# Optimization experiments

Measured on AMD Instinct MI355X. Metric: run time of the kernel, lower is better.

## Reference

```python
import jax, jax.numpy as jnp
import numpy as np

NUM_EXPERTS = 8
D_MODEL = 2048
D_FF = 4096
TOP_K = 2
NUM_TOKENS = 4096


def setup_inputs() -> dict:
    key = jax.random.key(0)
    k1, k2, k3, k4, k5, k6 = jax.random.split(key, 6)
    hidden_states = jax.random.normal(k1, (NUM_TOKENS, D_MODEL), dtype=jnp.float32)
    top_k_index = jax.random.randint(k2, (NUM_TOKENS, TOP_K), 0, NUM_EXPERTS)
    raw = jax.random.uniform(k3, (NUM_TOKENS, TOP_K), dtype=jnp.float32)
    top_k_weights = raw / jnp.sum(raw, axis=-1, keepdims=True)  # normalized router weights
    scale = 0.02
    Wg = jax.random.normal(k4, (NUM_EXPERTS, D_MODEL, D_FF), dtype=jnp.float32) * scale
    Wu = jax.random.normal(k5, (NUM_EXPERTS, D_MODEL, D_FF), dtype=jnp.float32) * scale
    Wd = jax.random.normal(k6, (NUM_EXPERTS, D_FF, D_MODEL), dtype=jnp.float32) * scale
    return {
        "hidden_states": hidden_states,
        "top_k_index": top_k_index,
        "top_k_weights": top_k_weights,
        "Wg": Wg,
        "Wu": Wu,
        "Wd": Wd,
    }


def reference(hidden_states, top_k_index, top_k_weights, Wg, Wu, Wd):
    T, D = hidden_states.shape
    E = Wg.shape[0]
    # Combine weights: [T, E], summing duplicate expert hits exactly as the
    # original loop's repeated index_add_ would.
    combine = jnp.zeros((T, E), dtype=top_k_weights.dtype)
    combine = combine.at[jnp.arange(T)[:, None], top_k_index].add(top_k_weights)
    # Dense all-experts SwiGLU (same math per token/expert as the gather loop)
    gate = jnp.einsum("td,edf->tef", hidden_states, Wg)   # [T, E, F]
    up = jnp.einsum("td,edf->tef", hidden_states, Wu)     # [T, E, F]
    h = jax.nn.silu(gate) * up                              # [T, E, F]
    expert_out = jnp.einsum("tef,efd->ted", h, Wd)          # [T, E, D]
    # Weighted scatter-combine
    final = jnp.einsum("ted,te->td", expert_out, combine)   # [T, D]
    return final
```

## Files before the change

kernel.cpp:

```cpp
#include <hip/hip_runtime.h>

#define NTOK 4096
#define DM   2048
#define DF   4096
#define NEXP 8

typedef __attribute__((ext_vector_type(4))) float f32x4;
typedef __attribute__((ext_vector_type(8))) short s16x8;
typedef __attribute__((ext_vector_type(4))) int   i32x4;

__device__ __forceinline__ unsigned short f2bf(float f) {
  union { float f; unsigned u; } x; x.f = f;
  unsigned r = x.u + 0x7fffu + ((x.u >> 16) & 1u);
  return (unsigned short)(r >> 16);
}

__device__ __forceinline__ int swz(int row, int ks) {
  return row * 32 + ((ks ^ ((row >> 1) & 3)) << 3);
}

__global__ void k_zero(int* counts, int* cursor) {
  int i = threadIdx.x;
  if (i < NEXP) { counts[i] = 0; cursor[i] = 0; }
}

__global__ void k_count(const int* __restrict__ idx, int* counts) {
  int t = blockIdx.x * 256 + threadIdx.x;
  if (t >= NTOK) return;
  int e0 = idx[2 * t], e1 = idx[2 * t + 1];
  atomicAdd(&counts[e0], 1);
  if (e1 != e0) atomicAdd(&counts[e1], 1);
}

__global__ void k_scan(const int* __restrict__ counts, int* offsets) {
  if (threadIdx.x == 0) {
    int s = 0;
    for (int e = 0; e < NEXP; e++) { offsets[e] = s; s += counts[e]; }
  }
}

__global__ void k_fill(const int* __restrict__ idx, const float* __restrict__ wts,
                       const int* __restrict__ offsets, int* cursor,
                       int* tokrow, float* wrow, int* rowids) {
  int t = blockIdx.x * 256 + threadIdx.x;
  if (t >= NTOK) return;
  int e0 = idx[2 * t], e1 = idx[2 * t + 1];
  float w0 = wts[2 * t], w1 = wts[2 * t + 1];
  if (e0 == e1) {
    int s = atomicAdd(&cursor[e0], 1);
    int g = offsets[e0] + s;
    tokrow[g] = t; wrow[g] = w0 + w1;
    rowids[2 * t] = g; rowids[2 * t + 1] = -1;
  } else {
    int s0 = atomicAdd(&cursor[e0], 1);
    int g0 = offsets[e0] + s0;
    tokrow[g0] = t; wrow[g0] = w0;
    int s1 = atomicAdd(&cursor[e1], 1);
    int g1 = offsets[e1] + s1;
    tokrow[g1] = t; wrow[g1] = w1;
    rowids[2 * t] = g0; rowids[2 * t + 1] = g1;
  }
}

__global__ __launch_bounds__(512, 2) void gemm1_kernel(
    const float* __restrict__ X, const float* __restrict__ Wg_all,
    const float* __restrict__ Wu_all, const int* __restrict__ counts,
    const int* __restrict__ offsets, const int* __restrict__ tokrow,
    unsigned short* __restrict__ H) {
  const int e = blockIdx.z;
  const int cnt = counts[e];
  const int m0 = blockIdx.y * 256;
  if (m0 >= cnt) return;
  const int n0 = blockIdx.x * 128;
  const int roff = offsets[e];
  const float* __restrict__ Wg = Wg_all + (size_t)e * DM * DF;
  const float* __restrict__ Wu = Wu_all + (size_t)e * DM * DF;

  __shared__ __attribute__((aligned(16))) short As[2][256 * 32];
  __shared__ __attribute__((aligned(16))) short Bs[2][2][128 * 32];

  const int tid = threadIdx.x;
  const int ar  = tid >> 1;
  const int aks = (tid & 1) * 2;
  const int am  = m0 + ar;
  const int atok = (am < cnt) ? tokrow[roff + am] : tokrow[roff];
  const float* __restrict__ xrow = X + (size_t)atok * DM + (tid & 1) * 16;
  const int bmat  = tid >> 8;
  const int bn    = tid & 127;
  const int bktop = ((tid >> 7) & 1) * 16;
  const float* __restrict__ wcol = (bmat ? Wu : Wg) + n0 + bn;

  const int wave = tid >> 6, lane = tid & 63;
  const int wm = wave >> 1, wn = wave & 1;
  const int lr = lane & 15, ks = lane >> 4;

  f32x4 accg[4][4], accu[4][4];
  #pragma unroll
  for (int i = 0; i < 4; i++)
    #pragma unroll
    for (int j = 0; j < 4; j++) {
      accg[i][j] = f32x4{0.f, 0.f, 0.f, 0.f};
      accu[i][j] = f32x4{0.f, 0.f, 0.f, 0.f};
    }

  auto stage = [&](int b, int k0) {
    const f32x4* ap = (const f32x4*)(xrow + k0);
    f32x4 a0 = ap[0], a1 = ap[1], a2 = ap[2], a3 = ap[3];
    float bv[16];
    const float* p = wcol + (size_t)(k0 + bktop) * DF;
    #pragma unroll
    for (int kk = 0; kk < 16; kk++) { bv[kk] = *p; p += DF; }
    s16x8 s;
    #pragma unroll
    for (int j = 0; j < 4; j++) { s[j] = (short)f2bf(a0[j]); s[4 + j] = (short)f2bf(a1[j]); }
    *(s16x8*)&As[b][swz(ar, aks)] = s;
    #pragma unroll
    for (int j = 0; j < 4; j++) { s[j] = (short)f2bf(a2[j]); s[4 + j] = (short)f2bf(a3[j]); }
    *(s16x8*)&As[b][swz(ar, aks + 1)] = s;
    #pragma unroll
    for (int j = 0; j < 8; j++) s[j] = (short)f2bf(bv[j]);
    *(s16x8*)&Bs[b][bmat][swz(bn, bktop >> 3)] = s;
    #pragma unroll
    for (int j = 0; j < 8; j++) s[j] = (short)f2bf(bv[8 + j]);
    *(s16x8*)&Bs[b][bmat][swz(bn, (bktop >> 3) + 1)] = s;
  };

  stage(0, 0);
  __syncthreads();
  int buf = 0;
  const int nK = DM / 32;
  for (int kt = 0; kt < nK; ++kt) {
    if (kt + 1 < nK) stage(buf ^ 1, (kt + 1) * 32);
    s16x8 af[4], bg[4], bu[4];
    #pragma unroll
    for (int mi = 0; mi < 4; mi++)
      af[mi] = *(const s16x8*)&As[buf][swz(wm * 64 + mi * 16 + lr, ks)];
    #pragma unroll
    for (int ni = 0; ni < 4; ni++) {
      bg[ni] = *(const s16x8*)&Bs[buf][0][swz(wn * 64 + ni * 16 + lr, ks)];
      bu[ni] = *(const s16x8*)&Bs[buf][1][swz(wn * 64 + ni * 16 + lr, ks)];
    }
    #pragma unroll
    for (int mi = 0; mi < 4; mi++)
      #pragma unroll
      for (int ni = 0; ni < 4; ni++) {
        accg[mi][ni] = __builtin_amdgcn_mfma_f32_16x16x32_bf16(af[mi], bg[ni], accg[mi][ni], 0, 0, 0);
        accu[mi][ni] = __builtin_amdgcn_mfma_f32_16x16x32_bf16(af[mi], bu[ni], accu[mi][ni], 0, 0, 0);
      }
    __syncthreads();
    buf ^= 1;
  }

  #pragma unroll
  for (int mi = 0; mi < 4; mi++) {
    #pragma unroll
    for (int r = 0; r < 4; r++) {
      int row = wm * 64 + mi * 16 + ks * 4 + r;
      if (m0 + row < cnt) {
        unsigned short* hrow = H + (size_t)(roff + m0 + row) * DF + n0 + wn * 64 + lr;
        #pragma unroll
        for (int ni = 0; ni < 4; ni++) {
          float g = accg[mi][ni][r], u = accu[mi][ni][r];
          float sv = g / (1.f + __expf(-g));
          hrow[ni * 16] = f2bf(sv * u);
        }
      }
    }
  }
}

__global__ __launch_bounds__(512, 2) void gemm2_kernel(
    const unsigned short* __restrict__ H, const float* __restrict__ Wd_all,
    const int* __restrict__ counts, const int* __restrict__ offsets,
    const float* __restrict__ wrow, float* __restrict__ OP) {
  const int e = blockIdx.z;
  const int cnt = counts[e];
  const int m0 = blockIdx.y * 256;
  if (m0 >= cnt) return;
  const int n0 = blockIdx.x * 128;
  const int roff = offsets[e];
  const float* __restrict__ Wd = Wd_all + (size_t)e * DF * DM;

  __shared__ __attribute__((aligned(16))) short As[2][256 * 32];
  __shared__ __attribute__((aligned(16))) short Bs[2][128 * 32];
  __shared__ float wl[256];

  const int tid = threadIdx.x;
  if (tid < 256) wl[tid] = (m0 + tid < cnt) ? wrow[roff + m0 + tid] : 0.f;

  const int ar  = tid >> 1;
  const int aks = (tid & 1) * 2;
  const int am  = m0 + ar;
  const int arow = (am < cnt) ? (roff + am) : roff;
  const unsigned short* __restrict__ hrow = H + (size_t)arow * DF + (tid & 1) * 16;

  const int bn  = tid & 127;
  const int bkg = tid >> 7;
  const float* __restrict__ wcol = Wd + n0 + bn;

  const int wave = tid >> 6, lane = tid & 63;
  const int wm = wave >> 1, wn = wave & 1;
  const int lr = lane & 15, ks = lane >> 4;

  f32x4 acc[4][4];
  #pragma unroll
  for (int i = 0; i < 4; i++)
    #pragma unroll
    for (int j = 0; j < 4; j++) acc[i][j] = f32x4{0.f, 0.f, 0.f, 0.f};

  auto stage = [&](int b, int k0) {
    const i32x4* ap = (const i32x4*)(hrow + k0);
    i32x4 h0 = ap[0], h1 = ap[1];
    float bv[8];
    const float* p = wcol + (size_t)(k0 + bkg * 8) * DM;
    #pragma unroll
    for (int kk = 0; kk < 8; kk++) { bv[kk] = *p; p += DM; }
    *(i32x4*)&As[b][swz(ar, aks)] = h0;
    *(i32x4*)&As[b][swz(ar, aks + 1)] = h1;
    s16x8 s;
    #pragma unroll
    for (int j = 0; j < 8; j++) s[j] = (short)f2bf(bv[j]);
    *(s16x8*)&Bs[b][swz(bn, bkg)] = s;
  };

  stage(0, 0);
  __syncthreads();
  int buf = 0;
  const int nK = DF / 32;
  for (int kt = 0; kt < nK; ++kt) {
    if (kt + 1 < nK) stage(buf ^ 1, (kt + 1) * 32);
    s16x8 af[4], bf_[4];
    #pragma unroll
    for (int mi = 0; mi < 4; mi++)
      af[mi] = *(const s16x8*)&As[buf][swz(wm * 64 + mi * 16 + lr, ks)];
    #pragma unroll
    for (int ni = 0; ni < 4; ni++)
      bf_[ni] = *(const s16x8*)&Bs[buf][swz(wn * 64 + ni * 16 + lr, ks)];
    #pragma unroll
    for (int mi = 0; mi < 4; mi++)
      #pragma unroll
      for (int ni = 0; ni < 4; ni++)
        acc[mi][ni] = __builtin_amdgcn_mfma_f32_16x16x32_bf16(af[mi], bf_[ni], acc[mi][ni], 0, 0, 0);
    __syncthreads();
    buf ^= 1;
  }

  #pragma unroll
  for (int mi = 0; mi < 4; mi++) {
    #pragma unroll
    for (int r = 0; r < 4; r++) {
      int row = wm * 64 + mi * 16 + ks * 4 + r;
      if (m0 + row < cnt) {
        float wgt = wl[row];
        float* orow = OP + (size_t)(roff + m0 + row) * DM + n0 + wn * 64 + lr;
        #pragma unroll
        for (int ni = 0; ni < 4; ni++) orow[ni * 16] = acc[mi][ni][r] * wgt;
      }
    }
  }
}

__global__ void k_combine(const float* __restrict__ OP, const int* __restrict__ rowids,
                          float* __restrict__ out) {
  int gid = blockIdx.x * 256 + threadIdx.x;
  if (gid >= NTOK * DM / 4) return;
  int t = gid >> 9;
  int c = (gid & 511) << 2;
  int r0 = rowids[2 * t], r1 = rowids[2 * t + 1];
  f32x4 v = *(const f32x4*)(OP + (size_t)r0 * DM + c);
  if (r1 >= 0) {
    f32x4 v1 = *(const f32x4*)(OP + (size_t)r1 * DM + c);
    v = v + v1;
  }
  *(f32x4*)(out + (size_t)t * DM + c) = v;
}

extern "C" void kernel_launch(void* const* d_in, const int* in_sizes, int n_in,
                              void* d_out, int out_size, void* d_ws, size_t ws_size,
                              hipStream_t stream) {
  (void)in_sizes; (void)n_in; (void)out_size; (void)ws_size;
  const float* X   = (const float*)d_in[0];
  const int*   idx = (const int*)d_in[1];
  const float* wts = (const float*)d_in[2];
  const float* Wg  = (const float*)d_in[3];
  const float* Wu  = (const float*)d_in[4];
  const float* Wd  = (const float*)d_in[5];
  float* out = (float*)d_out;

  uint8_t* w = (uint8_t*)d_ws;
  int*   counts  = (int*)(w + 0);
  int*   cursor  = (int*)(w + 64);
  int*   offsets = (int*)(w + 128);
  int*   tokrow  = (int*)(w + 256);
  float* wrow    = (float*)(w + 256 + 4 * 8192);
  int*   rowids  = (int*)(w + 256 + 8 * 8192);
  unsigned short* H = (unsigned short*)(w + 131072);
  float* OP = (float*)(w + 131072 + (size_t)8192 * DF * 2);

  k_zero<<<1, 64, 0, stream>>>(counts, cursor);
  k_count<<<16, 256, 0, stream>>>(idx, counts);
  k_scan<<<1, 64, 0, stream>>>(counts, offsets);
  k_fill<<<16, 256, 0, stream>>>(idx, wts, offsets, cursor, tokrow, wrow, rowids);
  gemm1_kernel<<<dim3(DF / 128, 16, NEXP), 512, 0, stream>>>(X, Wg, Wu, counts, offsets, tokrow, H);
  gemm2_kernel<<<dim3(DM / 128, 16, NEXP), 512, 0, stream>>>(H, Wd, counts, offsets, wrow, OP);
  k_combine<<<(NTOK * DM / 4) / 256, 256, 0, stream>>>(OP, rowids, out);
}
```

Measured before the change: 892.1 us.

## Pre-convert weights and gathered X to swizzled bf16 tiles, load via global_load_lds

```diff
diff --git a/kernel.cpp b/kernel.cpp
--- a/kernel.cpp
+++ b/kernel.cpp
@@ -1,26 +1,45 @@
 #include <hip/hip_runtime.h>
+#include <hip/hip_bf16.h>
+#include <stdint.h>
 
 #define NTOK 4096
 #define DM   2048
 #define DF   4096
 #define NEXP 8
+#define NPAD 10240
+#define NPTILE 40
 
 typedef __attribute__((ext_vector_type(4))) float f32x4;
 typedef __attribute__((ext_vector_type(8))) short s16x8;
 typedef __attribute__((ext_vector_type(4))) int   i32x4;
+typedef __attribute__((ext_vector_type(2))) int   i32x2;
 
 __device__ __forceinline__ unsigned short f2bf(float f) {
   union { float f; unsigned u; } x; x.f = f;
   unsigned r = x.u + 0x7fffu + ((x.u >> 16) & 1u);
   return (unsigned short)(r >> 16);
 }
-
+__device__ __forceinline__ unsigned pack2(float lo, float hi) {
+  __hip_bfloat162 h2 = __float22bfloat162_rn(make_float2(lo, hi));
+  return *reinterpret_cast<unsigned*>(&h2);
+}
 __device__ __forceinline__ int swz(int row, int ks) {
   return row * 32 + ((ks ^ ((row >> 1) & 3)) << 3);
 }
-
-__global__ void k_zero(int* counts, int* cursor) {
-  int i = threadIdx.x;
+__device__ __forceinline__ void g2l16(const void* g, void* l) {
+  __builtin_amdgcn_global_load_lds(
+      (const __attribute__((address_space(1))) void*)g,
+      (__attribute__((address_space(3))) void*)l, 16, 0, 0);
+}
+
+__global__ void k_zero_out(float* out) {
+  int gid = blockIdx.x * 256 + threadIdx.x;
+  *(f32x4*)(out + (size_t)gid * 4) = f32x4{0.f, 0.f, 0.f, 0.f};
+}
+
+__global__ void k_init(int* tokrow, int* counts, int* cursor) {
+  int i = blockIdx.x * 256 + threadIdx.x;
+  if (i < NPAD) tokrow[i] = 0;
   if (i < NEXP) { counts[i] = 0; cursor[i] = 0; }
 }
 
@@ -32,67 +51,103 @@
   if (e1 != e0) atomicAdd(&counts[e1], 1);
 }
 
-__global__ void k_scan(const int* __restrict__ counts, int* offsets) {
+__global__ void k_scan(const int* __restrict__ counts, int* poff) {
   if (threadIdx.x == 0) {
     int s = 0;
-    for (int e = 0; e < NEXP; e++) { offsets[e] = s; s += counts[e]; }
+    for (int e = 0; e < NEXP; e++) {
+      poff[e] = s;
+      s += ((counts[e] + 255) & ~255);
+    }
   }
 }
 
 __global__ void k_fill(const int* __restrict__ idx, const float* __restrict__ wts,
-                       const int* __restrict__ offsets, int* cursor,
-                       int* tokrow, float* wrow, int* rowids) {
+                       const int* __restrict__ poff, int* cursor,
+                       int* tokrow, float* wrow) {
   int t = blockIdx.x * 256 + threadIdx.x;
   if (t >= NTOK) return;
   int e0 = idx[2 * t], e1 = idx[2 * t + 1];
   float w0 = wts[2 * t], w1 = wts[2 * t + 1];
   if (e0 == e1) {
-    int s = atomicAdd(&cursor[e0], 1);
-    int g = offsets[e0] + s;
+    int g = poff[e0] + atomicAdd(&cursor[e0], 1);
     tokrow[g] = t; wrow[g] = w0 + w1;
-    rowids[2 * t] = g; rowids[2 * t + 1] = -1;
   } else {
-    int s0 = atomicAdd(&cursor[e0], 1);
-    int g0 = offsets[e0] + s0;
+    int g0 = poff[e0] + atomicAdd(&cursor[e0], 1);
     tokrow[g0] = t; wrow[g0] = w0;
-    int s1 = atomicAdd(&cursor[e1], 1);
-    int g1 = offsets[e1] + s1;
+    int g1 = poff[e1] + atomicAdd(&cursor[e1], 1);
     tokrow[g1] = t; wrow[g1] = w1;
-    rowids[2 * t] = g0; rowids[2 * t + 1] = g1;
-  }
+  }
+}
+
+__global__ void k_convX(const float* __restrict__ X, const int* __restrict__ tokrow,
+                        short* __restrict__ Xg) {
+  const int kt = blockIdx.x, tile = blockIdx.y, tid = threadIdx.x;
+  const int part = tid & 7;
+  short* dst = Xg + (size_t)(tile * 64 + kt) * 8192;
+  #pragma unroll
+  for (int it = 0; it < 8; it++) {
+    int row = it * 32 + (tid >> 3);
+    int tok = tokrow[tile * 256 + row];
+    f32x4 v = *(const f32x4*)(X + (size_t)tok * DM + kt * 32 + part * 4);
+    i32x2 p;
+    p[0] = (int)pack2(v[0], v[1]);
+    p[1] = (int)pack2(v[2], v[3]);
+    int idx = row * 32 + (((part >> 1) ^ ((row >> 1) & 3)) << 3) + (part & 1) * 4;
+    *(i32x2*)&dst[idx] = p;
+  }
+}
+
+__global__ void k_convW(const float* __restrict__ W_all, short* __restrict__ dstbuf,
+                        int e0, int N, int K) {
+  const int nt = blockIdx.x, kt = blockIdx.y, z = blockIdx.z;
+  const int e = e0 + z;
+  const int tid = threadIdx.x;
+  const int kl = tid >> 3, ng = (tid & 7) * 16;
+  const float* src = W_all + (size_t)e * K * N + (size_t)(kt * 32 + kl) * N + nt * 128 + ng;
+
+  __shared__ __attribute__((aligned(16))) short img[4096];
+
+  f32x4 v0 = ((const f32x4*)src)[0];
+  f32x4 v1 = ((const f32x4*)src)[1];
+  f32x4 v2 = ((const f32x4*)src)[2];
+  f32x4 v3 = ((const f32x4*)src)[3];
+  float vv[16];
+  *(f32x4*)&vv[0] = v0; *(f32x4*)&vv[4] = v1;
+  *(f32x4*)&vv[8] = v2; *(f32x4*)&vv[12] = v3;
+  const int ks = kl >> 3, kr = kl & 7;
+  #pragma unroll
+  for (int j = 0; j < 16; j++) {
+    int nl = ng + j;
+    img[nl * 32 + ((ks ^ ((nl >> 1) & 3)) << 3) + kr] = (short)f2bf(vv[j]);
+  }
+  __syncthreads();
+  short* dst = dstbuf + ((size_t)(z * (N / 128) + nt) * (K / 32) + kt) * 4096;
+  *(i32x4*)&dst[tid * 16]     = *(const i32x4*)&img[tid * 16];
+  *(i32x4*)&dst[tid * 16 + 8] = *(const i32x4*)&img[tid * 16 + 8];
 }
 
 __global__ __launch_bounds__(512, 2) void gemm1_kernel(
-    const float* __restrict__ X, const float* __restrict__ Wg_all,
-    const float* __restrict__ Wu_all, const int* __restrict__ counts,
-    const int* __restrict__ offsets, const int* __restrict__ tokrow,
-    unsigned short* __restrict__ H) {
-  const int e = blockIdx.z;
+    const short* __restrict__ Xg, const short* __restrict__ Wgt,
+    const short* __restrict__ Wut, const int* __restrict__ counts,
+    const int* __restrict__ poff, unsigned short* __restrict__ Hs, int e0) {
+  const int z = blockIdx.z, e = e0 + z;
   const int cnt = counts[e];
   const int m0 = blockIdx.y * 256;
   if (m0 >= cnt) return;
-  const int n0 = blockIdx.x * 128;
-  const int roff = offsets[e];
-  const float* __restrict__ Wg = Wg_all + (size_t)e * DM * DF;
-  const float* __restrict__ Wu = Wu_all + (size_t)e * DM * DF;
-
-  __shared__ __attribute__((aligned(16))) short As[2][256 * 32];
-  __shared__ __attribute__((aligned(16))) short Bs[2][2][128 * 32];
-
-  const int tid = threadIdx.x;
-  const int ar  = tid >> 1;
-  const int aks = (tid & 1) * 2;
-  const int am  = m0 + ar;
-  const int atok = (am < cnt) ? tokrow[roff + am] : tokrow[roff];
-  const float* __restrict__ xrow = X + (size_t)atok * DM + (tid & 1) * 16;
-  const int bmat  = tid >> 8;
-  const int bn    = tid & 127;
-  const int bktop = ((tid >> 7) & 1) * 16;
-  const float* __restrict__ wcol = (bmat ? Wu : Wg) + n0 + bn;
-
-  const int wave = tid >> 6, lane = tid & 63;
+  const int nt = blockIdx.x, n0 = nt * 128;
+  const int tileIdx = (poff[e] >> 8) + blockIdx.y;
+
+  __shared__ __attribute__((aligned(16))) short As[2][8192];
+  __shared__ __attribute__((aligned(16))) short Bs[2][2][4096];
+
+  const int tid = threadIdx.x, wave = tid >> 6, lane = tid & 63;
   const int wm = wave >> 1, wn = wave & 1;
   const int lr = lane & 15, ks = lane >> 4;
+  const int bmat = wave >> 2, wv = wave & 3;
+
+  const short* aS = Xg + (size_t)tileIdx * 64 * 8192 + wave * 1024 + lane * 8;
+  const short* bS = (bmat ? Wut : Wgt) + (size_t)(z * 32 + nt) * 64 * 4096
+                    + wv * 1024 + lane * 8;
 
   f32x4 accg[4][4], accu[4][4];
   #pragma unroll
@@ -103,26 +158,11 @@
       accu[i][j] = f32x4{0.f, 0.f, 0.f, 0.f};
     }
 
-  auto stage = [&](int b, int k0) {
-    const f32x4* ap = (const f32x4*)(xrow + k0);
-    f32x4 a0 = ap[0], a1 = ap[1], a2 = ap[2], a3 = ap[3];
-    float bv[16];
-    const float* p = wcol + (size_t)(k0 + bktop) * DF;
-    #pragma unroll
-    for (int kk = 0; kk < 16; kk++) { bv[kk] = *p; p += DF; }
-    s16x8 s;
-    #pragma unroll
-    for (int j = 0; j < 4; j++) { s[j] = (short)f2bf(a0[j]); s[4 + j] = (short)f2bf(a1[j]); }
-    *(s16x8*)&As[b][swz(ar, aks)] = s;
-    #pragma unroll
-    for (int j = 0; j < 4; j++) { s[j] = (short)f2bf(a2[j]); s[4 + j] = (short)f2bf(a3[j]); }
-    *(s16x8*)&As[b][swz(ar, aks + 1)] = s;
-    #pragma unroll
-    for (int j = 0; j < 8; j++) s[j] = (short)f2bf(bv[j]);
-    *(s16x8*)&Bs[b][bmat][swz(bn, bktop >> 3)] = s;
-    #pragma unroll
-    for (int j = 0; j < 8; j++) s[j] = (short)f2bf(bv[8 + j]);
-    *(s16x8*)&Bs[b][bmat][swz(bn, (bktop >> 3) + 1)] = s;
+  auto stage = [&](int b, int kt) {
+    g2l16(aS + (size_t)kt * 8192,       &As[b][wave * 1024]);
+    g2l16(aS + (size_t)kt * 8192 + 512, &As[b][wave * 1024 + 512]);
+    g2l16(bS + (size_t)kt * 4096,       &Bs[b][bmat][wv * 1024]);
+    g2l16(bS + (size_t)kt * 4096 + 512, &Bs[b][bmat][wv * 1024 + 512]);
   };
 
   stage(0, 0);
@@ -130,7 +170,7 @@
   int buf = 0;
   const int nK = DM / 32;
   for (int kt = 0; kt < nK; ++kt) {
-    if (kt + 1 < nK) stage(buf ^ 1, (kt + 1) * 32);
+    if (kt + 1 < nK) stage(buf ^ 1, kt + 1);
     s16x8 af[4], bg[4], bu[4];
     #pragma unroll
     for (int mi = 0; mi < 4; mi++)
@@ -151,18 +191,21 @@
     buf ^= 1;
   }
 
+  const size_t tb = (size_t)tileIdx * 128 * 8192;
   #pragma unroll
   for (int mi = 0; mi < 4; mi++) {
     #pragma unroll
     for (int r = 0; r < 4; r++) {
       int row = wm * 64 + mi * 16 + ks * 4 + r;
       if (m0 + row < cnt) {
-        unsigned short* hrow = H + (size_t)(roff + m0 + row) * DF + n0 + wn * 64 + lr;
         #pragma unroll
         for (int ni = 0; ni < 4; ni++) {
+          int col = n0 + wn * 64 + ni * 16 + lr;
           float g = accg[mi][ni][r], u = accu[mi][ni][r];
           float sv = g / (1.f + __expf(-g));
-          hrow[ni * 16] = f2bf(sv * u);
+          int ktH = col >> 5, kl = col & 31;
+          Hs[tb + (size_t)ktH * 8192 + row * 32 +
+             (((kl >> 3) ^ ((row >> 1) & 3)) << 3) + (kl & 7)] = f2bf(sv * u);
         }
       }
     }
@@ -170,57 +213,45 @@
 }
 
 __global__ __launch_bounds__(512, 2) void gemm2_kernel(
-    const unsigned short* __restrict__ H, const float* __restrict__ Wd_all,
-    const int* __restrict__ counts, const int* __restrict__ offsets,
-    const float* __restrict__ wrow, float* __restrict__ OP) {
-  const int e = blockIdx.z;
+    const unsigned short* __restrict__ Hs, const short* __restrict__ Wdt,
+    const int* __restrict__ counts, const int* __restrict__ poff,
+    const int* __restrict__ tokrow, const float* __restrict__ wrow,
+    float* __restrict__ out, int e0) {
+  const int z = blockIdx.z, e = e0 + z;
   const int cnt = counts[e];
   const int m0 = blockIdx.y * 256;
   if (m0 >= cnt) return;
-  const int n0 = blockIdx.x * 128;
-  const int roff = offsets[e];
-  const float* __restrict__ Wd = Wd_all + (size_t)e * DF * DM;
-
-  __shared__ __attribute__((aligned(16))) short As[2][256 * 32];
-  __shared__ __attribute__((aligned(16))) short Bs[2][128 * 32];
+  const int nt = blockIdx.x, n0 = nt * 128;
+  const int tileIdx = (poff[e] >> 8) + blockIdx.y;
+
+  __shared__ __attribute__((aligned(16))) short As[2][8192];
+  __shared__ __attribute__((aligned(16))) short Bs[2][4096];
   __shared__ float wl[256];
-
-  const int tid = threadIdx.x;
-  if (tid < 256) wl[tid] = (m0 + tid < cnt) ? wrow[roff + m0 + tid] : 0.f;
-
-  const int ar  = tid >> 1;
-  const int aks = (tid & 1) * 2;
-  const int am  = m0 + ar;
-  const int arow = (am < cnt) ? (roff + am) : roff;
-  const unsigned short* __restrict__ hrow = H + (size_t)arow * DF + (tid & 1) * 16;
-
-  const int bn  = tid & 127;
-  const int bkg = tid >> 7;
-  const float* __restrict__ wcol = Wd + n0 + bn;
-
-  const int wave = tid >> 6, lane = tid & 63;
+  __shared__ int   tl[256];
+
+  const int tid = threadIdx.x, wave = tid >> 6, lane = tid & 63;
   const int wm = wave >> 1, wn = wave & 1;
   const int lr = lane & 15, ks = lane >> 4;
 
+  if (tid < 256) {
+    int rp = poff[e] + m0 + tid;
+    wl[tid] = wrow[rp];
+    tl[tid] = tokrow[rp];
+  }
+
+  const unsigned short* aS = Hs + (size_t)tileIdx * 128 * 8192 + wave * 1024 + lane * 8;
+  const short* bS = Wdt + (size_t)(z * 16 + nt) * 128 * 4096 + wave * 512 + lane * 8;
+
   f32x4 acc[4][4];
   #pragma unroll
   for (int i = 0; i < 4; i++)
     #pragma unroll
     for (int j = 0; j < 4; j++) acc[i][j] = f32x4{0.f, 0.f, 0.f, 0.f};
 
-  auto stage = [&](int b, int k0) {
-    const i32x4* ap = (const i32x4*)(hrow + k0);
-    i32x4 h0 = ap[0], h1 = ap[1];
-    float bv[8];
-    const float* p = wcol + (size_t)(k0 + bkg * 8) * DM;
-    #pragma unroll
-    for (int kk = 0; kk < 8; kk++) { bv[kk] = *p; p += DM; }
-    *(i32x4*)&As[b][swz(ar, aks)] = h0;
-    *(i32x4*)&As[b][swz(ar, aks + 1)] = h1;
-    s16x8 s;
-    #pragma unroll
-    for (int j = 0; j < 8; j++) s[j] = (short)f2bf(bv[j]);
-    *(s16x8*)&Bs[b][swz(bn, bkg)] = s;
+  auto stage = [&](int b, int kt) {
+    g2l16(aS + (size_t)kt * 8192,       &As[b][wave * 1024]);
+    g2l16(aS + (size_t)kt * 8192 + 512, &As[b][wave * 1024 + 512]);
+    g2l16(bS + (size_t)kt * 4096,       &Bs[b][wave * 512]);
   };
 
   stage(0, 0);
@@ -228,7 +259,7 @@
   int buf = 0;
   const int nK = DF / 32;
   for (int kt = 0; kt < nK; ++kt) {
-    if (kt + 1 < nK) stage(buf ^ 1, (kt + 1) * 32);
+    if (kt + 1 < nK) stage(buf ^ 1, kt + 1);
     s16x8 af[4], bf_[4];
     #pragma unroll
     for (int mi = 0; mi < 4; mi++)
@@ -252,27 +283,13 @@
       int row = wm * 64 + mi * 16 + ks * 4 + r;
       if (m0 + row < cnt) {
         float wgt = wl[row];
-        float* orow = OP + (size_t)(roff + m0 + row) * DM + n0 + wn * 64 + lr;
+        float* obase = out + (size_t)tl[row] * DM + n0 + wn * 64 + lr;
         #pragma unroll
-        for (int ni = 0; ni < 4; ni++) orow[ni * 16] = acc[mi][ni][r] * wgt;
+        for (int ni = 0; ni < 4; ni++)
+          atomicAdd(obase + ni * 16, acc[mi][ni][r] * wgt);
       }
     }
   }
-}
-
-__global__ void k_combine(const float* __restrict__ OP, const int* __restrict__ rowids,
-                          float* __restrict__ out) {
-  int gid = blockIdx.x * 256 + threadIdx.x;
-  if (gid >= NTOK * DM / 4) return;
-  int t = gid >> 9;
-  int c = (gid & 511) << 2;
-  int r0 = rowids[2 * t], r1 = rowids[2 * t + 1];
-  f32x4 v = *(const f32x4*)(OP + (size_t)r0 * DM + c);
-  if (r1 >= 0) {
-    f32x4 v1 = *(const f32x4*)(OP + (size_t)r1 * DM + c);
-    v = v + v1;
-  }
-  *(f32x4*)(out + (size_t)t * DM + c) = v;
 }
 
 extern "C" void kernel_launch(void* const* d_in, const int* in_sizes, int n_in,
@@ -288,20 +305,33 @@
   float* out = (float*)d_out;
 
   uint8_t* w = (uint8_t*)d_ws;
-  int*   counts  = (int*)(w + 0);
-  int*   cursor  = (int*)(w + 64);
-  int*   offsets = (int*)(w + 128);
-  int*   tokrow  = (int*)(w + 256);
-  float* wrow    = (float*)(w + 256 + 4 * 8192);
-  int*   rowids  = (int*)(w + 256 + 8 * 8192);
-  unsigned short* H = (unsigned short*)(w + 131072);
-  float* OP = (float*)(w + 131072 + (size_t)8192 * DF * 2);
-
-  k_zero<<<1, 64, 0, stream>>>(counts, cursor);
+  int*   counts = (int*)(w + 0);
+  int*   cursor = (int*)(w + 64);
+  int*   poff   = (int*)(w + 128);
+  int*   tokrow = (int*)(w + 4096);
+  float* wrow   = (float*)(w + 45056);
+  short* Xg     = (short*)(w + (1ull << 20));
+  unsigned short* Hs = (unsigned short*)(w + (48ull << 20));
+  short* Wgt    = (short*)(w + (132ull << 20));
+  short* Wut    = (short*)(w + (166ull << 20));
+  short* Wdt    = (short*)(w + (132ull << 20));
+
+  k_zero_out<<<NTOK * DM / 1024, 256, 0, stream>>>(out);
+  k_init<<<NPTILE, 256, 0, stream>>>(tokrow, counts, cursor);
   k_count<<<16, 256, 0, stream>>>(idx, counts);
-  k_scan<<<1, 64, 0, stream>>>(counts, offsets);
-  k_fill<<<16, 256, 0, stream>>>(idx, wts, offsets, cursor, tokrow, wrow, rowids);
-  gemm1_kernel<<<dim3(DF / 128, 16, NEXP), 512, 0, stream>>>(X, Wg, Wu, counts, offsets, tokrow, H);
-  gemm2_kernel<<<dim3(DM / 128, 16, NEXP), 512, 0, stream>>>(H, Wd, counts, offsets, wrow, OP);
-  k_combine<<<(NTOK * DM / 4) / 256, 256, 0, stream>>>(OP, rowids, out);
-}
+  k_scan<<<1, 64, 0, stream>>>(counts, poff);
+  k_fill<<<16, 256, 0, stream>>>(idx, wts, poff, cursor, tokrow, wrow);
+  k_convX<<<dim3(DM / 32, NPTILE), 256, 0, stream>>>(X, tokrow, Xg);
+
+  for (int p = 0; p < 4; p++) {
+    int e0 = 2 * p;
+    k_convW<<<dim3(DF / 128, DM / 32, 2), 256, 0, stream>>>(Wg, Wgt, e0, DF, DM);
+    k_convW<<<dim3(DF / 128, DM / 32, 2), 256, 0, stream>>>(Wu, Wut, e0, DF, DM);
+    gemm1_kernel<<<dim3(DF / 128, 16, 2), 512, 0, stream>>>(Xg, Wgt, Wut, counts, poff, Hs, e0);
+  }
+  for (int p = 0; p < 4; p++) {
+    int e0 = 2 * p;
+    k_convW<<<dim3(DM / 128, DF / 32, 2), 256, 0, stream>>>(Wd, Wdt, e0, DM, DF);
+    gemm2_kernel<<<dim3(DM / 128, 16, 2), 512, 0, stream>>>(Hs, Wdt, counts, poff, tokrow, wrow, out, e0);
+  }
+}
```

Result: slower. 1.246 ms (+39.7%).
